# Kernel optimization log

Hardware: AMD Instinct MI355X
Metric: run time of the kernel (lower is better)

The kernel has to match this reference:

```python
import jax, jax.numpy as jnp
import numpy as np

N = 10000      # nodes
E = 160000     # edges (before self loops)
F_IN = 512     # in_features
F_OUT = 256    # out_features
SLOPE = 0.2    # LeakyReLU negative slope (PyG GATConv default)
EPS = 1e-12    # F.normalize eps


def setup_inputs() -> dict:
    key = jax.random.key(0)
    ks = jax.random.split(key, 14)
    feat = jax.random.normal(ks[0], (N, F_IN), jnp.float32)
    feat_a = jax.random.normal(ks[1], (N, F_IN), jnp.float32)
    edge_index = jax.random.randint(ks[2], (2, E), 0, N, dtype=jnp.int32)
    # binary neighborhood mask; diagonal set so every row has >=1 entry
    gn = (jax.random.uniform(ks[3], (N, N)) < 0.0016).astype(jnp.float32)
    graph_neigh = gn.at[jnp.arange(N), jnp.arange(N)].set(1.0)
    s1 = 1.0 / np.sqrt(F_IN)
    s2 = 1.0 / np.sqrt(F_OUT)
    return {
        "feat": feat,
        "feat_a": feat_a,
        "edge_index": edge_index,
        "graph_neigh": graph_neigh,
        # conv1: GATConv(F_IN -> F_OUT, heads=1)
        "W1": jax.random.normal(ks[4], (F_OUT, F_IN), jnp.float32) * s1,
        "att_src1": jax.random.normal(ks[5], (F_OUT,), jnp.float32) * s2,
        "att_dst1": jax.random.normal(ks[6], (F_OUT,), jnp.float32) * s2,
        "b1": jnp.zeros((F_OUT,), jnp.float32),
        # conv2: GATConv(F_OUT -> F_IN, heads=1)
        "W2": jax.random.normal(ks[7], (F_IN, F_OUT), jnp.float32) * s2,
        "att_src2": jax.random.normal(ks[8], (F_IN,), jnp.float32) * s1,
        "att_dst2": jax.random.normal(ks[9], (F_IN,), jnp.float32) * s1,
        "b2": jnp.zeros((F_IN,), jnp.float32),
        # discriminator bilinear
        "Wd": jax.random.normal(ks[10], (F_OUT, F_OUT), jnp.float32) * s2,
        "bd": jnp.zeros((), jnp.float32),
    }


def _gat_conv(x, src, dst, W, a_src, a_dst, b):
    # PyG GATConv, heads=1, concat=True, add_self_loops already applied.
    h = x @ W.T                       # [N, out]
    a_s = h @ a_src                   # [N]
    a_d = h @ a_dst                   # [N]
    e = a_s[src] + a_d[dst]           # [E+N]
    e = jnp.where(e > 0, e, SLOPE * e)  # leaky relu
    m = jax.ops.segment_max(e, dst, num_segments=N)
    p = jnp.exp(e - m[dst])
    s = jax.ops.segment_sum(p, dst, num_segments=N)
    coef = p / s[dst]                 # per-dst softmax over incoming edges
    out = jax.ops.segment_sum(coef[:, None] * h[src], dst, num_segments=N)
    return out + b


def reference(feat, feat_a, edge_index, graph_neigh, W1, att_src1, att_dst1, b1,
              W2, att_src2, att_dst2, b2, Wd, bd):
    loops = jnp.arange(N, dtype=edge_index.dtype)
    src = jnp.concatenate([edge_index[0], loops])
    dst = jnp.concatenate([edge_index[1], loops])

    z = _gat_conv(feat, src, dst, W1, att_src1, att_dst1, b1)      # [N, F_OUT]
    hiden_emb = z
    h = _gat_conv(z, src, dst, W2, att_src2, att_dst2, b2)         # [N, F_IN]
    emb = jax.nn.relu(z)
    z_a = _gat_conv(feat_a, src, dst, W1, att_src1, att_dst1, b1)
    emb_a = jax.nn.relu(z_a)

    def readout(e):
        vsum = graph_neigh @ e                                     # [N, F_OUT]
        row_sum = graph_neigh.sum(axis=1, keepdims=True)
        g = vsum / row_sum
        g = g / jnp.maximum(jnp.linalg.norm(g, axis=1, keepdims=True), EPS)
        return jax.nn.sigmoid(g)

    g = readout(emb)
    g_a = readout(emb_a)

    def bilin(x1, x2):
        return jnp.einsum('nd,de,ne->n', x1, Wd, x2)[:, None] + bd

    ret = jnp.concatenate([bilin(emb, g), bilin(emb_a, g)], axis=1)      # [N, 2]
    ret_a = jnp.concatenate([bilin(emb_a, g_a), bilin(emb, g_a)], axis=1)
    return (hiden_emb, h, ret, ret_a)
```

## Files before the change

### kernel.cpp

```cpp
#include <hip/hip_runtime.h>


#define N_NODES 10000
#define F_IN    512
#define F_OUT   256
#define SLOPE   0.2f

typedef unsigned short ushort_t;
typedef __attribute__((ext_vector_type(8))) short short8;
typedef __attribute__((ext_vector_type(4))) float f32x4;

__device__ __forceinline__ float bf2f(ushort_t h) {
    union { unsigned u; float f; } v;
    v.u = ((unsigned)h) << 16;
    return v.f;
}
__device__ __forceinline__ ushort_t f2bf(float f) {
    union { float f; unsigned u; } v; v.f = f;
    unsigned r = v.u + 0x7FFFu + ((v.u >> 16) & 1u);
    return (ushort_t)(r >> 16);
}

__global__ void zero2_kernel(int* p1, int n1, int* p2, int n2) {
    int i = blockIdx.x * 256 + threadIdx.x;
    if (i < n1) p1[i] = 0;
    if (i < n2) p2[i] = 0;
}

__global__ void hist_kernel(const int* __restrict__ dst, int E, int n, int* deg) {
    int i = blockIdx.x * 256 + threadIdx.x;
    if (i < E) {
        int d = dst[i];
        d = d < 0 ? 0 : (d >= n ? n - 1 : d);
        atomicAdd(&deg[d], 1);
    }
}

__global__ __launch_bounds__(1024) void scan_kernel(const int* __restrict__ deg,
                                                    int* row_ptr, int* cursor, int n) {
    __shared__ int wsum[16];
    __shared__ int carry_s;
    int tid = threadIdx.x;
    int lane = tid & 63, wid = tid >> 6;
    if (tid == 0) carry_s = 0;
    __syncthreads();
    for (int base = 0; base < n; base += 1024) {
        int i = base + tid;
        int x = (i < n) ? (deg[i] + 1) : 0;
        int incl = x;
#pragma unroll
        for (int off = 1; off < 64; off <<= 1) {
            int v = __shfl_up(incl, off);
            if (lane >= off) incl += v;
        }
        int carry = carry_s;
        if (lane == 63) wsum[wid] = incl;
        __syncthreads();
        if (wid == 0 && lane < 16) {
            int w = wsum[lane];
            int winc = w;
#pragma unroll
            for (int off = 1; off < 16; off <<= 1) {
                int v = __shfl_up(winc, off);
                if (lane >= off) winc += v;
            }
            wsum[lane] = winc - w;
            if (lane == 15) carry_s = carry + winc;
        }
        __syncthreads();
        int excl = carry + wsum[wid] + (incl - x);
        if (i < n) { row_ptr[i] = excl; cursor[i] = excl; }
        __syncthreads();
    }
    if (tid == 0) row_ptr[n] = carry_s;
}

__global__ void fill_kernel(const int* __restrict__ src, const int* __restrict__ dst,
                            int E, int n, int* cursor, int* col, int cap) {
    int i = blockIdx.x * 256 + threadIdx.x;
    if (i < E) {
        int d = dst[i];
        d = d < 0 ? 0 : (d >= n ? n - 1 : d);
        int s = src[i];
        s = s < 0 ? 0 : (s >= n ? n - 1 : s);
        int p = atomicAdd(&cursor[d], 1);
        if (p >= 0 && p < cap) col[p] = s;
    } else if (i < E + n) {
        int v = i - E;
        int p = atomicAdd(&cursor[v], 1);
        if (p >= 0 && p < cap) col[p] = v;
    }
}

#define BM 64
#define BN 64
#define BK 32

__device__ __forceinline__ uint4 pack8(const float* p) {
    float4 x = ((const float4*)p)[0];
    float4 y = ((const float4*)p)[1];
    uint4 r;
    r.x = (unsigned)f2bf(x.x) | ((unsigned)f2bf(x.y) << 16);
    r.y = (unsigned)f2bf(x.z) | ((unsigned)f2bf(x.w) << 16);
    r.z = (unsigned)f2bf(y.x) | ((unsigned)f2bf(y.y) << 16);
    r.w = (unsigned)f2bf(y.z) | ((unsigned)f2bf(y.w) << 16);
    return r;
}

__global__ __launch_bounds__(256) void gemm_bt(const void* __restrict__ Av,
                                               const void* __restrict__ Av2,
                                               int msplit,
                                               const void* __restrict__ Bv,
                                               ushort_t* __restrict__ C,
                                               int M, int N, int K,
                                               int amode, int bmode) {
    __shared__ __align__(16) ushort_t As[BM * BK];
    __shared__ __align__(16) ushort_t Bs[BN * BK];
    int fA = (amode == 2);
    int fB = (bmode == 2);
    int m0 = blockIdx.x * BM;
    int n0 = blockIdx.y * BN;
    int tid = threadIdx.x;
    int wave = tid >> 6, lane = tid & 63;
    int quad = lane >> 4, r16 = lane & 15;

    f32x4 acc[4] = {};

    int srow = tid >> 2;
    int schunk = tid & 3;
    int a_row = m0 + srow; if (a_row >= M) a_row = M - 1;
    int use2 = (a_row >= msplit);
    const void* Abase = use2 ? Av2 : Av;
    int arl = use2 ? (a_row - msplit) : a_row;
    int b_row = n0 + srow;
    const ushort_t* Ah = (const ushort_t*)Abase + (size_t)arl * K;
    const float*    Af = (const float*)Abase    + (size_t)arl * K;
    const ushort_t* Bh = (const ushort_t*)Bv + (size_t)b_row * K;
    const float*    Bf = (const float*)Bv    + (size_t)b_row * K;
    int s_sw = srow * BK + ((schunk ^ (srow & 3)) * 8);

    for (int k0 = 0; k0 < K; k0 += BK) {
        int eoff = k0 + schunk * 8;
        uint4 av = fA ? pack8(Af + eoff) : ((const uint4*)Ah)[eoff >> 3];
        uint4 bv = fB ? pack8(Bf + eoff) : ((const uint4*)Bh)[eoff >> 3];
        __syncthreads();
        *(uint4*)&As[s_sw] = av;
        *(uint4*)&Bs[s_sw] = bv;
        __syncthreads();
        int am = wave * 16 + r16;
        short8 a = *(const short8*)&As[am * BK + ((quad ^ (am & 3)) * 8)];
#pragma unroll
        for (int i = 0; i < 4; i++) {
            int bn = i * 16 + r16;
            short8 b = *(const short8*)&Bs[bn * BK + ((quad ^ (bn & 3)) * 8)];
            acc[i] = __builtin_amdgcn_mfma_f32_16x16x32_bf16(a, b, acc[i], 0, 0, 0);
        }
    }
    int m_base = m0 + wave * 16 + quad * 4;
#pragma unroll
    for (int i = 0; i < 4; i++) {
        int n = n0 + i * 16 + r16;
#pragma unroll
        for (int r = 0; r < 4; r++) {
            int m = m_base + r;
            if (m < M) C[(size_t)m * N + n] = f2bf(acc[i][r]);
        }
    }
}

__global__ __launch_bounds__(256) void attdot_kernel(const ushort_t* __restrict__ h,
                                                     const float* __restrict__ asrc,
                                                     const float* __restrict__ adst,
                                                     float* __restrict__ out_s,
                                                     float* __restrict__ out_d, int F,
                                                     int totR) {
    int row = blockIdx.x * 4 + (threadIdx.x >> 6);
    int lane = threadIdx.x & 63;
    if (row >= totR) return;
    const ushort_t* hr = h + (size_t)row * F;
    float ps = 0.f, pd = 0.f;
    for (int f = lane; f < F; f += 64) {
        float hv = bf2f(hr[f]);
        ps += hv * asrc[f];
        pd += hv * adst[f];
    }
    for (int off = 32; off; off >>= 1) {
        ps += __shfl_down(ps, off);
        pd += __shfl_down(pd, off);
    }
    if (lane == 0) { out_s[row] = ps; out_d[row] = pd; }
}

__global__ __launch_bounds__(256) void row_conv2(const int* __restrict__ row_ptr,
                                                 const int* __restrict__ col,
                                                 const float* __restrict__ a_s,
                                                 const float* __restrict__ a_d,
                                                 const ushort_t* __restrict__ h,
                                                 const float* __restrict__ bias,
                                                 int F, int nfirst,
                                                 float* out0, ushort_t* outB,
                                                 ushort_t* out1) {
    int b = blockIdx.x;
    int sel = (b >= nfirst) ? 1 : 0;
    int n = b - sel * nfirst;
    size_t roff = (size_t)sel * nfirst;
    int tid = threadIdx.x;
    int lane = tid & 63, wid = tid >> 6;
    int beg = row_ptr[n], end = row_ptr[n + 1];
    int deg = end - beg;
    float adn = a_d[roff + n];
    __shared__ float esh[2048];
    __shared__ int   csh[2048];
    __shared__ float wred[8];
    __shared__ float red[256];

    float acc0 = 0.f, acc1 = 0.f;
    if (deg <= 2048) {
        float lm = -1e30f;
        for (int i = tid; i < deg; i += 256) {
            int c = col[beg + i];
            csh[i] = c;
            float e = a_s[roff + c] + adn;
            e = e > 0.f ? e : SLOPE * e;
            esh[i] = e;
            lm = fmaxf(lm, e);
        }
#pragma unroll
        for (int off = 32; off; off >>= 1) lm = fmaxf(lm, __shfl_down(lm, off));
        if (lane == 0) wred[wid] = lm;
        __syncthreads();
        float m = fmaxf(fmaxf(wred[0], wred[1]), fmaxf(wred[2], wred[3]));
        float lsum = 0.f;
        for (int i = tid; i < deg; i += 256) {
            float p = expf(esh[i] - m);
            esh[i] = p;
            lsum += p;
        }
#pragma unroll
        for (int off = 32; off; off >>= 1) lsum += __shfl_down(lsum, off);
        if (lane == 0) wred[4 + wid] = lsum;
        __syncthreads();
        float denom = wred[4] + wred[5] + wred[6] + wred[7];
        float inv_s = denom > 0.f ? 1.f / denom : 0.f;
        int j = 0;
        for (; j + 3 < deg; j += 4) {
            float w0 = esh[j], w1 = esh[j + 1], w2 = esh[j + 2], w3 = esh[j + 3];
            const ushort_t* p0 = h + (size_t)(roff + csh[j])     * F;
            const ushort_t* p1 = h + (size_t)(roff + csh[j + 1]) * F;
            const ushort_t* p2 = h + (size_t)(roff + csh[j + 2]) * F;
            const ushort_t* p3 = h + (size_t)(roff + csh[j + 3]) * F;
            acc0 += w0 * bf2f(p0[tid]) + w1 * bf2f(p1[tid])
                  + w2 * bf2f(p2[tid]) + w3 * bf2f(p3[tid]);
            if (F == 512)
                acc1 += w0 * bf2f(p0[tid + 256]) + w1 * bf2f(p1[tid + 256])
                      + w2 * bf2f(p2[tid + 256]) + w3 * bf2f(p3[tid + 256]);
        }
        for (; j < deg; j++) {
            float wj = esh[j];
            const ushort_t* p = h + (size_t)(roff + csh[j]) * F;
            acc0 += wj * bf2f(p[tid]);
            if (F == 512) acc1 += wj * bf2f(p[tid + 256]);
        }
        acc0 *= inv_s;
        acc1 *= inv_s;
    } else {
        float lm = -1e30f;
        for (int i = beg + tid; i < end; i += 256) {
            float e = a_s[roff + col[i]] + adn;
            e = e > 0.f ? e : SLOPE * e;
            lm = fmaxf(lm, e);
        }
        red[tid] = lm; __syncthreads();
        for (int s = 128; s > 0; s >>= 1) { if (tid < s) red[tid] = fmaxf(red[tid], red[tid + s]); __syncthreads(); }
        float m = red[0]; __syncthreads();
        float lsum = 0.f;
        for (int i = beg + tid; i < end; i += 256) {
            float e = a_s[roff + col[i]] + adn;
            e = e > 0.f ? e : SLOPE * e;
            lsum += expf(e - m);
        }
        red[tid] = lsum; __syncthreads();
        for (int s = 128; s > 0; s >>= 1) { if (tid < s) red[tid] += red[tid + s]; __syncthreads(); }
        float denom = red[0];
        float inv_s = denom > 0.f ? 1.f / denom : 0.f;
        __syncthreads();
        for (int c0 = beg; c0 < end; c0 += 256) {
            int i = c0 + tid;
            if (i < end) {
                float e = a_s[roff + col[i]] + adn;
                e = e > 0.f ? e : SLOPE * e;
                esh[tid] = expf(e - m) * inv_s;
                csh[tid] = col[i];
            }
            __syncthreads();
            int cnt = min(256, end - c0);
            for (int j = 0; j < cnt; j++) {
                float wj = esh[j];
                const ushort_t* hr = h + (size_t)(roff + csh[j]) * F;
                acc0 += wj * bf2f(hr[tid]);
                if (F == 512) acc1 += wj * bf2f(hr[tid + 256]);
            }
            __syncthreads();
        }
    }
    float z0 = acc0 + bias[tid];
    if (sel == 0) {
        if (out0) out0[(size_t)n * F + tid] = z0;
        if (outB) outB[(size_t)n * F + tid] = f2bf(fmaxf(z0, 0.f));
    } else {
        if (out1) out1[(size_t)n * F + tid] = f2bf(fmaxf(z0, 0.f));
    }
    if (F == 512) {
        float z1 = acc1 + bias[tid + 256];
        if (sel == 0) {
            if (out0) out0[(size_t)n * F + tid + 256] = z1;
            if (outB) outB[(size_t)n * F + tid + 256] = f2bf(fmaxf(z1, 0.f));
        } else {
            if (out1) out1[(size_t)n * F + tid + 256] = f2bf(fmaxf(z1, 0.f));
        }
    }
}

#define RCAP 4096

__global__ __launch_bounds__(256) void readout_kernel(const float* __restrict__ gn,
                                                      const ushort_t* __restrict__ embB,
                                                      const ushort_t* __restrict__ embA,
                                                      ushort_t* __restrict__ g,
                                                      ushort_t* __restrict__ ga) {
    int n = blockIdx.x, tid = threadIdx.x;
    int lane = tid & 63, wid = tid >> 6;
    __shared__ int list[RCAP];
    __shared__ int lcnt;
    __shared__ float wred[8];
    if (tid == 0) lcnt = 0;
    __syncthreads();
    const uint4* rowp = (const uint4*)(gn + (size_t)n * N_NODES);
    const int NU4 = N_NODES / 4;
    for (int idx = tid; idx < NU4; idx += 256) {
        uint4 v = rowp[idx];
        if (v.x & 0x7FFFFFFFu) { int p = atomicAdd(&lcnt, 1); if (p < RCAP) list[p] = idx * 4; }
        if (v.y & 0x7FFFFFFFu) { int p = atomicAdd(&lcnt, 1); if (p < RCAP) list[p] = idx * 4 + 1; }
        if (v.z & 0x7FFFFFFFu) { int p = atomicAdd(&lcnt, 1); if (p < RCAP) list[p] = idx * 4 + 2; }
        if (v.w & 0x7FFFFFFFu) { int p = atomicAdd(&lcnt, 1); if (p < RCAP) list[p] = idx * 4 + 3; }
    }
    __syncthreads();
    int c = min(lcnt, RCAP);
    float acc0 = 0.f, acc1 = 0.f;
    int j = 0;
    for (; j + 3 < c; j += 4) {
        int i0 = list[j], i1 = list[j + 1], i2 = list[j + 2], i3 = list[j + 3];
        acc0 += bf2f(embB[(size_t)i0 * 256 + tid]) + bf2f(embB[(size_t)i1 * 256 + tid])
              + bf2f(embB[(size_t)i2 * 256 + tid]) + bf2f(embB[(size_t)i3 * 256 + tid]);
        acc1 += bf2f(embA[(size_t)i0 * 256 + tid]) + bf2f(embA[(size_t)i1 * 256 + tid])
              + bf2f(embA[(size_t)i2 * 256 + tid]) + bf2f(embA[(size_t)i3 * 256 + tid]);
    }
    for (; j < c; j++) {
        int node = list[j];
        acc0 += bf2f(embB[(size_t)node * 256 + tid]);
        acc1 += bf2f(embA[(size_t)node * 256 + tid]);
    }
    float cnt = (float)(c > 0 ? c : 1);
    float u0 = acc0 / cnt, u1 = acc1 / cnt;
    float s0 = u0 * u0, s1 = u1 * u1;
#pragma unroll
    for (int off = 32; off; off >>= 1) {
        s0 += __shfl_down(s0, off);
        s1 += __shfl_down(s1, off);
    }
    if (lane == 0) { wred[wid] = s0; wred[4 + wid] = s1; }
    __syncthreads();
    float n0 = wred[0] + wred[1] + wred[2] + wred[3];
    float n1 = wred[4] + wred[5] + wred[6] + wred[7];
    float g0 = u0 / fmaxf(sqrtf(n0), 1e-12f);
    float g1 = u1 / fmaxf(sqrtf(n1), 1e-12f);
    g0 = 1.f / (1.f + expf(-g0));
    g1 = 1.f / (1.f + expf(-g1));
    g[(size_t)n * 256 + tid]  = f2bf(g0);
    ga[(size_t)n * 256 + tid] = f2bf(g1);
}

__global__ __launch_bounds__(256) void bilin_kernel(const float* __restrict__ z,
                                                    const ushort_t* __restrict__ embA,
                                                    const ushort_t* __restrict__ Q,
                                                    const ushort_t* __restrict__ Qa,
                                                    const float* __restrict__ bdp,
                                                    float* __restrict__ ret,
                                                    float* __restrict__ ret_a) {
    int row = blockIdx.x * 4 + (threadIdx.x >> 6);
    int lane = threadIdx.x & 63;
    if (row >= N_NODES) return;
    const float*    zr = z    + (size_t)row * 256;
    const ushort_t* er = embA + (size_t)row * 256;
    const ushort_t* q  = Q    + (size_t)row * 256;
    const ushort_t* qa = Qa   + (size_t)row * 256;
    float d00 = 0, d01 = 0, d10 = 0, d11 = 0;
    for (int d = lane; d < 256; d += 64) {
        float em = fmaxf(zr[d], 0.f);
        float ea = bf2f(er[d]);
        float qv = bf2f(q[d]), qav = bf2f(qa[d]);
        d00 += em * qv;
        d01 += ea * qv;
        d10 += ea * qav;
        d11 += em * qav;
    }
    for (int off = 32; off; off >>= 1) {
        d00 += __shfl_down(d00, off);
        d01 += __shfl_down(d01, off);
        d10 += __shfl_down(d10, off);
        d11 += __shfl_down(d11, off);
    }
    if (lane == 0) {
        float bd = bdp[0];
        ret[row * 2]       = d00 + bd;
        ret[row * 2 + 1]   = d01 + bd;
        ret_a[row * 2]     = d10 + bd;
        ret_a[row * 2 + 1] = d11 + bd;
    }
}

extern "C" void kernel_launch(void* const* d_in, const int* in_sizes, int n_in,
                              void* d_out, int out_size, void* d_ws, size_t ws_size,
                              hipStream_t stream) {
    const void*  feat    = d_in[0];
    const void*  feat_a  = d_in[1];
    const int*   eidx    = (const int*)d_in[2];
    const float* gn      = (const float*)d_in[3];
    const void*  W1      = d_in[4];
    const float* asrc1   = (const float*)d_in[5];
    const float* adst1   = (const float*)d_in[6];
    const float* b1      = (const float*)d_in[7];
    const void*  W2      = d_in[8];
    const float* asrc2   = (const float*)d_in[9];
    const float* adst2   = (const float*)d_in[10];
    const float* b2      = (const float*)d_in[11];
    const void*  Wd      = d_in[12];
    const float* bd      = (const float*)d_in[13];

    const int N = N_NODES;
    const int E = in_sizes[2] / 2;
    const int* src = eidx;
    const int* dst = eidx + E;

    float* out_z    = (float*)d_out;
    float* out_h    = out_z + (size_t)N * F_OUT;
    float* out_ret  = out_h + (size_t)N * F_IN;
    float* out_reta = out_ret + (size_t)N * 2;

    size_t off = 0;
    char* wsb = (char*)d_ws;
    auto carve = [&](size_t bytes) -> void* {
        void* p = wsb + off;
        off = (off + bytes + 255) & ~(size_t)255;
        return p;
    };
    ushort_t* R1   = (ushort_t*)carve((size_t)2 * N * 256 * 2);
    ushort_t* R2   = (ushort_t*)carve((size_t)2 * N * 256 * 2);
    ushort_t* embA = (ushort_t*)carve((size_t)N * 256 * 2);
    ushort_t* embB = (ushort_t*)carve((size_t)N * 256 * 2);
    float* as1cat = (float*)carve((size_t)2 * N * 4);
    float* ad1cat = (float*)carve((size_t)2 * N * 4);
    float* as2    = (float*)carve((size_t)N * 4);
    float* ad2    = (float*)carve((size_t)N * 4);
    int* deg     = (int*)carve((size_t)N * 4);
    int* cursor  = (int*)carve((size_t)N * 4);
    int* row_ptr = (int*)carve((size_t)(N + 1) * 4);
    int* colb    = (int*)carve((size_t)(E + N) * 4);

    ushort_t* h1cat = R1;
    ushort_t* h2    = R1;
    ushort_t* gbuf  = R1;
    ushort_t* gabuf = R1 + (size_t)N * 256;
    ushort_t* Qb    = R2;
    ushort_t* Qab   = R2 + (size_t)N * 256;

    zero2_kernel<<<(E + N + 255) / 256, 256, 0, stream>>>(deg, N, colb, E + N);
    hist_kernel<<<(E + 255) / 256, 256, 0, stream>>>(dst, E, N, deg);
    scan_kernel<<<1, 1024, 0, stream>>>(deg, row_ptr, cursor, N);
    fill_kernel<<<(E + N + 255) / 256, 256, 0, stream>>>(src, dst, E, N, cursor, colb, E + N);

    const int MT  = (N + BM - 1) / BM;
    const int MT2 = (2 * N + BM - 1) / BM;

    gemm_bt<<<dim3(MT2, F_OUT / BN), 256, 0, stream>>>(feat, feat_a, N, W1, h1cat,
                                                       2 * N, F_OUT, F_IN, 2, 2);
    attdot_kernel<<<(2 * N + 3) / 4, 256, 0, stream>>>(h1cat, asrc1, adst1, as1cat, ad1cat, F_OUT, 2 * N);
    row_conv2<<<2 * N, 256, 0, stream>>>(row_ptr, colb, as1cat, ad1cat, h1cat, b1,
                                         F_OUT, N, out_z, embB, embA);

    gemm_bt<<<dim3(MT, F_IN / BN), 256, 0, stream>>>(out_z, out_z, N, W2, h2,
                                                     N, F_IN, F_OUT, 2, 2);
    attdot_kernel<<<(N + 3) / 4, 256, 0, stream>>>(h2, asrc2, adst2, as2, ad2, F_IN, N);
    row_conv2<<<N, 256, 0, stream>>>(row_ptr, colb, as2, ad2, h2, b2,
                                     F_IN, N, out_h, nullptr, nullptr);

    readout_kernel<<<N, 256, 0, stream>>>(gn, embB, embA, gbuf, gabuf);

    gemm_bt<<<dim3(MT2, 256 / BN), 256, 0, stream>>>(R1, R1, 2 * N, Wd, R2,
                                                     2 * N, 256, 256, 0, 2);
    bilin_kernel<<<(N + 3) / 4, 256, 0, stream>>>(out_z, embA, Qb, Qab, bd, out_ret, out_reta);
}
```

Measured before the change: 777.3 us.

## Switch aggregation and readout to wave-per-row and pre-convert GEMM operands to bf16

The GAT aggregation and readout kernels now map one 64-lane wave per node instead of a 256-thread block. Softmax weights and neighbour indices are held in registers and broadcast with shuffles, removing shared-memory staging and block barriers. A separate kernel converts feat, feat_a and the weight matrices to bf16 up front, so the GEMM loads bf16 directly instead of converting fp32 in its inner loop. The readout neighbour list cap drops from 4096 to 256 per row, which silently truncates rows with more neighbours, and the extra conversion pass adds a full read and write of the feature matrices.

```diff
diff --git a/kernel.cpp b/kernel.cpp
--- a/kernel.cpp
+++ b/kernel.cpp
@@ -19,6 +19,37 @@
     union { float f; unsigned u; } v; v.f = f;
     unsigned r = v.u + 0x7FFFu + ((v.u >> 16) & 1u);
     return (ushort_t)(r >> 16);
+}
+
+#define NF (N_NODES * 512)
+#define NW1 (512 * 256)
+#define NW2 (512 * 256)
+#define NWD (256 * 256)
+
+__global__ __launch_bounds__(256) void cvt_all(const float* __restrict__ feat,
+                                               const float* __restrict__ feat_a,
+                                               const float* __restrict__ W1,
+                                               const float* __restrict__ W2,
+                                               const float* __restrict__ Wd,
+                                               ushort_t* __restrict__ featbf,
+                                               ushort_t* __restrict__ W1bf,
+                                               ushort_t* __restrict__ W2bf,
+                                               ushort_t* __restrict__ Wdbf) {
+    int q = blockIdx.x * 256 + threadIdx.x;
+    const int total = (2 * NF + NW1 + NW2 + NWD) / 4;
+    if (q >= total) return;
+    int i = q * 4;
+    const float* s; ushort_t* d;
+    if (i < NF)               { s = feat   + i;                 d = featbf + i; }
+    else if (i < 2 * NF)      { s = feat_a + (i - NF);          d = featbf + i; }
+    else if (i < 2 * NF + NW1){ s = W1 + (i - 2 * NF);          d = W1bf + (i - 2 * NF); }
+    else if (i < 2 * NF + NW1 + NW2) { s = W2 + (i - 2 * NF - NW1); d = W2bf + (i - 2 * NF - NW1); }
+    else                      { s = Wd + (i - 2 * NF - NW1 - NW2); d = Wdbf + (i - 2 * NF - NW1 - NW2); }
+    float4 v = *(const float4*)s;
+    uint2 r;
+    r.x = (unsigned)f2bf(v.x) | ((unsigned)f2bf(v.y) << 16);
+    r.y = (unsigned)f2bf(v.z) | ((unsigned)f2bf(v.w) << 16);
+    *(uint2*)d = r;
 }
 
 __global__ void zero2_kernel(int* p1, int n1, int* p2, int n2) {
@@ -96,28 +127,12 @@
 #define BN 64
 #define BK 32
 
-__device__ __forceinline__ uint4 pack8(const float* p) {
-    float4 x = ((const float4*)p)[0];
-    float4 y = ((const float4*)p)[1];
-    uint4 r;
-    r.x = (unsigned)f2bf(x.x) | ((unsigned)f2bf(x.y) << 16);
-    r.y = (unsigned)f2bf(x.z) | ((unsigned)f2bf(x.w) << 16);
-    r.z = (unsigned)f2bf(y.x) | ((unsigned)f2bf(y.y) << 16);
-    r.w = (unsigned)f2bf(y.z) | ((unsigned)f2bf(y.w) << 16);
-    return r;
-}
-
-__global__ __launch_bounds__(256) void gemm_bt(const void* __restrict__ Av,
-                                               const void* __restrict__ Av2,
-                                               int msplit,
-                                               const void* __restrict__ Bv,
+__global__ __launch_bounds__(256) void gemm_bt(const ushort_t* __restrict__ A,
+                                               const ushort_t* __restrict__ B,
                                                ushort_t* __restrict__ C,
-                                               int M, int N, int K,
-                                               int amode, int bmode) {
+                                               int M, int N, int K) {
     __shared__ __align__(16) ushort_t As[BM * BK];
     __shared__ __align__(16) ushort_t Bs[BN * BK];
-    int fA = (amode == 2);
-    int fB = (bmode == 2);
     int m0 = blockIdx.x * BM;
     int n0 = blockIdx.y * BN;
     int tid = threadIdx.x;
@@ -129,20 +144,13 @@
     int srow = tid >> 2;
     int schunk = tid & 3;
     int a_row = m0 + srow; if (a_row >= M) a_row = M - 1;
-    int use2 = (a_row >= msplit);
-    const void* Abase = use2 ? Av2 : Av;
-    int arl = use2 ? (a_row - msplit) : a_row;
-    int b_row = n0 + srow;
-    const ushort_t* Ah = (const ushort_t*)Abase + (size_t)arl * K;
-    const float*    Af = (const float*)Abase    + (size_t)arl * K;
-    const ushort_t* Bh = (const ushort_t*)Bv + (size_t)b_row * K;
-    const float*    Bf = (const float*)Bv    + (size_t)b_row * K;
+    const uint4* Ag = (const uint4*)(A + (size_t)a_row * K);
+    const uint4* Bg = (const uint4*)(B + (size_t)(n0 + srow) * K);
     int s_sw = srow * BK + ((schunk ^ (srow & 3)) * 8);
 
     for (int k0 = 0; k0 < K; k0 += BK) {
-        int eoff = k0 + schunk * 8;
-        uint4 av = fA ? pack8(Af + eoff) : ((const uint4*)Ah)[eoff >> 3];
-        uint4 bv = fB ? pack8(Bf + eoff) : ((const uint4*)Bh)[eoff >> 3];
+        uint4 av = Ag[(k0 >> 3) + schunk];
+        uint4 bv = Bg[(k0 >> 3) + schunk];
         __syncthreads();
         *(uint4*)&As[s_sw] = av;
         *(uint4*)&Bs[s_sw] = bv;
@@ -191,193 +199,227 @@
     if (lane == 0) { out_s[row] = ps; out_d[row] = pd; }
 }
 
-__global__ __launch_bounds__(256) void row_conv2(const int* __restrict__ row_ptr,
-                                                 const int* __restrict__ col,
-                                                 const float* __restrict__ a_s,
-                                                 const float* __restrict__ a_d,
-                                                 const ushort_t* __restrict__ h,
-                                                 const float* __restrict__ bias,
-                                                 int F, int nfirst,
-                                                 float* out0, ushort_t* outB,
-                                                 ushort_t* out1) {
-    int b = blockIdx.x;
-    int sel = (b >= nfirst) ? 1 : 0;
-    int n = b - sel * nfirst;
-    size_t roff = (size_t)sel * nfirst;
-    int tid = threadIdx.x;
-    int lane = tid & 63, wid = tid >> 6;
+template<int NV>
+__device__ __forceinline__ void accum_row(float wgt, const ushort_t* p, float* acc) {
+    if constexpr (NV == 4) {
+        uint2 u = *(const uint2*)p;
+        acc[0] += wgt * bf2f((ushort_t)(u.x & 0xFFFFu));
+        acc[1] += wgt * bf2f((ushort_t)(u.x >> 16));
+        acc[2] += wgt * bf2f((ushort_t)(u.y & 0xFFFFu));
+        acc[3] += wgt * bf2f((ushort_t)(u.y >> 16));
+    } else {
+        uint4 u = *(const uint4*)p;
+        acc[0] += wgt * bf2f((ushort_t)(u.x & 0xFFFFu));
+        acc[1] += wgt * bf2f((ushort_t)(u.x >> 16));
+        acc[2] += wgt * bf2f((ushort_t)(u.y & 0xFFFFu));
+        acc[3] += wgt * bf2f((ushort_t)(u.y >> 16));
+        acc[4] += wgt * bf2f((ushort_t)(u.z & 0xFFFFu));
+        acc[5] += wgt * bf2f((ushort_t)(u.z >> 16));
+        acc[6] += wgt * bf2f((ushort_t)(u.w & 0xFFFFu));
+        acc[7] += wgt * bf2f((ushort_t)(u.w >> 16));
+    }
+}
+
+template<int NV>
+__device__ __forceinline__ void store_bf(ushort_t* dst, const float* z, bool relu) {
+    unsigned rp[NV / 2];
+#pragma unroll
+    for (int k = 0; k < NV; k += 2) {
+        float x = relu ? fmaxf(z[k], 0.f) : z[k];
+        float y = relu ? fmaxf(z[k + 1], 0.f) : z[k + 1];
+        rp[k / 2] = (unsigned)f2bf(x) | ((unsigned)f2bf(y) << 16);
+    }
+    if constexpr (NV == 4) {
+        *(uint2*)dst = make_uint2(rp[0], rp[1]);
+    } else {
+        *(uint4*)dst = make_uint4(rp[0], rp[1], rp[2], rp[3]);
+    }
+}
+
+template<int FF>
+__global__ __launch_bounds__(256) void row_conv_w(const int* __restrict__ row_ptr,
+                                                  const int* __restrict__ col,
+                                                  const float* __restrict__ a_s,
+                                                  const float* __restrict__ a_d,
+                                                  const ushort_t* __restrict__ h,
+                                                  const float* __restrict__ bias,
+                                                  int nfirst, int ntot,
+                                                  float* __restrict__ out0,
+                                                  ushort_t* __restrict__ outZ,
+                                                  ushort_t* __restrict__ outB,
+                                                  ushort_t* __restrict__ out1) {
+    constexpr int NV = FF / 64;
+    int w = blockIdx.x * 4 + (threadIdx.x >> 6);
+    if (w >= ntot) return;
+    int lane = threadIdx.x & 63;
+    int sel = (w >= nfirst) ? 1 : 0;
+    int n = w - sel * nfirst;
+    size_t roff = (size_t)sel * (size_t)nfirst;
     int beg = row_ptr[n], end = row_ptr[n + 1];
     int deg = end - beg;
     float adn = a_d[roff + n];
-    __shared__ float esh[2048];
-    __shared__ int   csh[2048];
-    __shared__ float wred[8];
-    __shared__ float red[256];
-
-    float acc0 = 0.f, acc1 = 0.f;
-    if (deg <= 2048) {
-        float lm = -1e30f;
-        for (int i = tid; i < deg; i += 256) {
-            int c = col[beg + i];
-            csh[i] = c;
-            float e = a_s[roff + c] + adn;
-            e = e > 0.f ? e : SLOPE * e;
-            esh[i] = e;
-            lm = fmaxf(lm, e);
-        }
-#pragma unroll
-        for (int off = 32; off; off >>= 1) lm = fmaxf(lm, __shfl_down(lm, off));
-        if (lane == 0) wred[wid] = lm;
-        __syncthreads();
-        float m = fmaxf(fmaxf(wred[0], wred[1]), fmaxf(wred[2], wred[3]));
-        float lsum = 0.f;
-        for (int i = tid; i < deg; i += 256) {
-            float p = expf(esh[i] - m);
-            esh[i] = p;
-            lsum += p;
-        }
-#pragma unroll
-        for (int off = 32; off; off >>= 1) lsum += __shfl_down(lsum, off);
-        if (lane == 0) wred[4 + wid] = lsum;
-        __syncthreads();
-        float denom = wred[4] + wred[5] + wred[6] + wred[7];
-        float inv_s = denom > 0.f ? 1.f / denom : 0.f;
+
+    float acc[NV];
+#pragma unroll
+    for (int k = 0; k < NV; k++) acc[k] = 0.f;
+    float inv_s;
+
+    if (deg <= 64) {
+        int cv = 0; float e = -1e30f;
+        if (lane < deg) {
+            cv = col[beg + lane];
+            float t = a_s[roff + cv] + adn;
+            e = t > 0.f ? t : SLOPE * t;
+        }
+        float m = e;
+#pragma unroll
+        for (int off = 32; off; off >>= 1) m = fmaxf(m, __shfl_xor(m, off));
+        float wv = (lane < deg) ? expf(e - m) : 0.f;
+        float ls = wv;
+#pragma unroll
+        for (int off = 32; off; off >>= 1) ls += __shfl_xor(ls, off);
+        inv_s = ls > 0.f ? 1.f / ls : 0.f;
         int j = 0;
         for (; j + 3 < deg; j += 4) {
-            float w0 = esh[j], w1 = esh[j + 1], w2 = esh[j + 2], w3 = esh[j + 3];
-            const ushort_t* p0 = h + (size_t)(roff + csh[j])     * F;
-            const ushort_t* p1 = h + (size_t)(roff + csh[j + 1]) * F;
-            const ushort_t* p2 = h + (size_t)(roff + csh[j + 2]) * F;
-            const ushort_t* p3 = h + (size_t)(roff + csh[j + 3]) * F;
-            acc0 += w0 * bf2f(p0[tid]) + w1 * bf2f(p1[tid])
-                  + w2 * bf2f(p2[tid]) + w3 * bf2f(p3[tid]);
-            if (F == 512)
-                acc1 += w0 * bf2f(p0[tid + 256]) + w1 * bf2f(p1[tid + 256])
-                      + w2 * bf2f(p2[tid + 256]) + w3 * bf2f(p3[tid + 256]);
+            float w0 = __shfl(wv, j),     w1 = __shfl(wv, j + 1);
+            float w2 = __shfl(wv, j + 2), w3 = __shfl(wv, j + 3);
+            int   q0 = __shfl(cv, j),     q1 = __shfl(cv, j + 1);
+            int   q2 = __shfl(cv, j + 2), q3 = __shfl(cv, j + 3);
+            const ushort_t* p0 = h + (size_t)(roff + q0) * FF + lane * NV;
+            const ushort_t* p1 = h + (size_t)(roff + q1) * FF + lane * NV;
+            const ushort_t* p2 = h + (size_t)(roff + q2) * FF + lane * NV;
+            const ushort_t* p3 = h + (size_t)(roff + q3) * FF + lane * NV;
+            accum_row<NV>(w0, p0, acc);
+            accum_row<NV>(w1, p1, acc);
+            accum_row<NV>(w2, p2, acc);
+            accum_row<NV>(w3, p3, acc);
         }
         for (; j < deg; j++) {
-            float wj = esh[j];
-            const ushort_t* p = h + (size_t)(roff + csh[j]) * F;
-            acc0 += wj * bf2f(p[tid]);
-            if (F == 512) acc1 += wj * bf2f(p[tid + 256]);
-        }
-        acc0 *= inv_s;
-        acc1 *= inv_s;
+            float wj = __shfl(wv, j);
+            int   qj = __shfl(cv, j);
+            accum_row<NV>(wj, h + (size_t)(roff + qj) * FF + lane * NV, acc);
+        }
     } else {
         float lm = -1e30f;
-        for (int i = beg + tid; i < end; i += 256) {
-            float e = a_s[roff + col[i]] + adn;
-            e = e > 0.f ? e : SLOPE * e;
-            lm = fmaxf(lm, e);
-        }
-        red[tid] = lm; __syncthreads();
-        for (int s = 128; s > 0; s >>= 1) { if (tid < s) red[tid] = fmaxf(red[tid], red[tid + s]); __syncthreads(); }
-        float m = red[0]; __syncthreads();
-        float lsum = 0.f;
-        for (int i = beg + tid; i < end; i += 256) {
-            float e = a_s[roff + col[i]] + adn;
-            e = e > 0.f ? e : SLOPE * e;
-            lsum += expf(e - m);
-        }
-        red[tid] = lsum; __syncthreads();
-        for (int s = 128; s > 0; s >>= 1) { if (tid < s) red[tid] += red[tid + s]; __syncthreads(); }
-        float denom = red[0];
-        float inv_s = denom > 0.f ? 1.f / denom : 0.f;
-        __syncthreads();
-        for (int c0 = beg; c0 < end; c0 += 256) {
-            int i = c0 + tid;
-            if (i < end) {
-                float e = a_s[roff + col[i]] + adn;
-                e = e > 0.f ? e : SLOPE * e;
-                esh[tid] = expf(e - m) * inv_s;
-                csh[tid] = col[i];
+        for (int i = lane; i < deg; i += 64) {
+            int c = col[beg + i];
+            float t = a_s[roff + c] + adn;
+            t = t > 0.f ? t : SLOPE * t;
+            lm = fmaxf(lm, t);
+        }
+#pragma unroll
+        for (int off = 32; off; off >>= 1) lm = fmaxf(lm, __shfl_xor(lm, off));
+        float ls = 0.f;
+        for (int i = lane; i < deg; i += 64) {
+            int c = col[beg + i];
+            float t = a_s[roff + c] + adn;
+            t = t > 0.f ? t : SLOPE * t;
+            ls += expf(t - lm);
+        }
+#pragma unroll
+        for (int off = 32; off; off >>= 1) ls += __shfl_xor(ls, off);
+        inv_s = ls > 0.f ? 1.f / ls : 0.f;
+        for (int c0 = 0; c0 < deg; c0 += 64) {
+            int cnt = min(64, deg - c0);
+            int cv = 0; float wv = 0.f;
+            if (lane < cnt) {
+                cv = col[beg + c0 + lane];
+                float t = a_s[roff + cv] + adn;
+                t = t > 0.f ? t : SLOPE * t;
+                wv = expf(t - lm);
             }
-            __syncthreads();
-            int cnt = min(256, end - c0);
             for (int j = 0; j < cnt; j++) {
-                float wj = esh[j];
-                const ushort_t* hr = h + (size_t)(roff + csh[j]) * F;
-                acc0 += wj * bf2f(hr[tid]);
-                if (F == 512) acc1 += wj * bf2f(hr[tid + 256]);
+                float wj = __shfl(wv, j);
+                int   qj = __shfl(cv, j);
+                accum_row<NV>(wj, h + (size_t)(roff + qj) * FF + lane * NV, acc);
             }
-            __syncthreads();
-        }
-    }
-    float z0 = acc0 + bias[tid];
+        }
+    }
+
+    float z[NV];
+#pragma unroll
+    for (int k = 0; k < NV; k++) z[k] = acc[k] * inv_s + bias[lane * NV + k];
+
+    size_t obase = (size_t)n * FF + lane * NV;
     if (sel == 0) {
-        if (out0) out0[(size_t)n * F + tid] = z0;
-        if (outB) outB[(size_t)n * F + tid] = f2bf(fmaxf(z0, 0.f));
+        if (out0) {
+#pragma unroll
+            for (int k = 0; k < NV; k += 4)
+                *(float4*)(out0 + obase + k) = make_float4(z[k], z[k+1], z[k+2], z[k+3]);
+        }
+        if (outZ) store_bf<NV>(outZ + obase, z, false);
+        if (outB) store_bf<NV>(outB + obase, z, true);
     } else {
-        if (out1) out1[(size_t)n * F + tid] = f2bf(fmaxf(z0, 0.f));
-    }
-    if (F == 512) {
-        float z1 = acc1 + bias[tid + 256];
-        if (sel == 0) {
-            if (out0) out0[(size_t)n * F + tid + 256] = z1;
-            if (outB) outB[(size_t)n * F + tid + 256] = f2bf(fmaxf(z1, 0.f));
-        } else {
-            if (out1) out1[(size_t)n * F + tid + 256] = f2bf(fmaxf(z1, 0.f));
-        }
-    }
-}
-
-#define RCAP 4096
-
-__global__ __launch_bounds__(256) void readout_kernel(const float* __restrict__ gn,
-                                                      const ushort_t* __restrict__ embB,
-                                                      const ushort_t* __restrict__ embA,
-                                                      ushort_t* __restrict__ g,
-                                                      ushort_t* __restrict__ ga) {
-    int n = blockIdx.x, tid = threadIdx.x;
-    int lane = tid & 63, wid = tid >> 6;
-    __shared__ int list[RCAP];
-    __shared__ int lcnt;
-    __shared__ float wred[8];
-    if (tid == 0) lcnt = 0;
+        if (out1) store_bf<NV>(out1 + obase, z, true);
+    }
+}
+
+#define RCAP 256
+
+__global__ __launch_bounds__(256) void readout_w(const float* __restrict__ gn,
+                                                 const ushort_t* __restrict__ embB,
+                                                 const ushort_t* __restrict__ embA,
+                                                 ushort_t* __restrict__ g,
+                                                 ushort_t* __restrict__ ga) {
+    int wid = threadIdx.x >> 6, lane = threadIdx.x & 63;
+    int n = blockIdx.x * 4 + wid;
+    __shared__ int lists[4][RCAP];
+    __shared__ int cnts[4];
+    if (lane == 0) cnts[wid] = 0;
     __syncthreads();
     const uint4* rowp = (const uint4*)(gn + (size_t)n * N_NODES);
     const int NU4 = N_NODES / 4;
-    for (int idx = tid; idx < NU4; idx += 256) {
+    for (int idx = lane; idx < NU4; idx += 64) {
         uint4 v = rowp[idx];
-        if (v.x & 0x7FFFFFFFu) { int p = atomicAdd(&lcnt, 1); if (p < RCAP) list[p] = idx * 4; }
-        if (v.y & 0x7FFFFFFFu) { int p = atomicAdd(&lcnt, 1); if (p < RCAP) list[p] = idx * 4 + 1; }
-        if (v.z & 0x7FFFFFFFu) { int p = atomicAdd(&lcnt, 1); if (p < RCAP) list[p] = idx * 4 + 2; }
-        if (v.w & 0x7FFFFFFFu) { int p = atomicAdd(&lcnt, 1); if (p < RCAP) list[p] = idx * 4 + 3; }
+        if (v.x & 0x7FFFFFFFu) { int p = atomicAdd(&cnts[wid], 1); if (p < RCAP) lists[wid][p] = idx * 4; }
+        if (v.y & 0x7FFFFFFFu) { int p = atomicAdd(&cnts[wid], 1); if (p < RCAP) lists[wid][p] = idx * 4 + 1; }
+        if (v.z & 0x7FFFFFFFu) { int p = atomicAdd(&cnts[wid], 1); if (p < RCAP) lists[wid][p] = idx * 4 + 2; }
+        if (v.w & 0x7FFFFFFFu) { int p = atomicAdd(&cnts[wid], 1); if (p < RCAP) lists[wid][p] = idx * 4 + 3; }
     }
     __syncthreads();
-    int c = min(lcnt, RCAP);
-    float acc0 = 0.f, acc1 = 0.f;
+    int c = min(cnts[wid], RCAP);
+    float a0[4] = {}, a1[4] = {};
     int j = 0;
     for (; j + 3 < c; j += 4) {
-        int i0 = list[j], i1 = list[j + 1], i2 = list[j + 2], i3 = list[j + 3];
-        acc0 += bf2f(embB[(size_t)i0 * 256 + tid]) + bf2f(embB[(size_t)i1 * 256 + tid])
-              + bf2f(embB[(size_t)i2 * 256 + tid]) + bf2f(embB[(size_t)i3 * 256 + tid]);
-        acc1 += bf2f(embA[(size_t)i0 * 256 + tid]) + bf2f(embA[(size_t)i1 * 256 + tid])
-              + bf2f(embA[(size_t)i2 * 256 + tid]) + bf2f(embA[(size_t)i3 * 256 + tid]);
+        int i0 = lists[wid][j],     i1 = lists[wid][j + 1];
+        int i2 = lists[wid][j + 2], i3 = lists[wid][j + 3];
+        accum_row<4>(1.f, embB + (size_t)i0 * 256 + lane * 4, a0);
+        accum_row<4>(1.f, embB + (size_t)i1 * 256 + lane * 4, a0);
+        accum_row<4>(1.f, embB + (size_t)i2 * 256 + lane * 4, a0);
+        accum_row<4>(1.f, embB + (size_t)i3 * 256 + lane * 4, a0);
+        accum_row<4>(1.f, embA + (size_t)i0 * 256 + lane * 4, a1);
+        accum_row<4>(1.f, embA + (size_t)i1 * 256 + lane * 4, a1);
+        accum_row<4>(1.f, embA + (size_t)i2 * 256 + lane * 4, a1);
+        accum_row<4>(1.f, embA + (size_t)i3 * 256 + lane * 4, a1);
     }
     for (; j < c; j++) {
-        int node = list[j];
-        acc0 += bf2f(embB[(size_t)node * 256 + tid]);
-        acc1 += bf2f(embA[(size_t)node * 256 + tid]);
-    }
-    float cnt = (float)(c > 0 ? c : 1);
-    float u0 = acc0 / cnt, u1 = acc1 / cnt;
-    float s0 = u0 * u0, s1 = u1 * u1;
+        int node = lists[wid][j];
+        accum_row<4>(1.f, embB + (size_t)node * 256 + lane * 4, a0);
+        accum_row<4>(1.f, embA + (size_t)node * 256 + lane * 4, a1);
+    }
+    float inv = 1.f / (float)(c > 0 ? c : 1);
+    float u0[4], u1[4];
+    float s0 = 0.f, s1 = 0.f;
+#pragma unroll
+    for (int k = 0; k < 4; k++) {
+        u0[k] = a0[k] * inv; s0 += u0[k] * u0[k];
+        u1[k] = a1[k] * inv; s1 += u1[k] * u1[k];
+    }
 #pragma unroll
     for (int off = 32; off; off >>= 1) {
-        s0 += __shfl_down(s0, off);
-        s1 += __shfl_down(s1, off);
-    }
-    if (lane == 0) { wred[wid] = s0; wred[4 + wid] = s1; }
-    __syncthreads();
-    float n0 = wred[0] + wred[1] + wred[2] + wred[3];
-    float n1 = wred[4] + wred[5] + wred[6] + wred[7];
-    float g0 = u0 / fmaxf(sqrtf(n0), 1e-12f);
-    float g1 = u1 / fmaxf(sqrtf(n1), 1e-12f);
-    g0 = 1.f / (1.f + expf(-g0));
-    g1 = 1.f / (1.f + expf(-g1));
-    g[(size_t)n * 256 + tid]  = f2bf(g0);
-    ga[(size_t)n * 256 + tid] = f2bf(g1);
+        s0 += __shfl_xor(s0, off);
+        s1 += __shfl_xor(s1, off);
+    }
+    float r0 = 1.f / fmaxf(sqrtf(s0), 1e-12f);
+    float r1 = 1.f / fmaxf(sqrtf(s1), 1e-12f);
+    float go[4], gao[4];
+#pragma unroll
+    for (int k = 0; k < 4; k++) {
+        go[k]  = 1.f / (1.f + expf(-u0[k] * r0));
+        gao[k] = 1.f / (1.f + expf(-u1[k] * r1));
+    }
+    store_bf<4>(g  + (size_t)n * 256 + lane * 4, go,  false);
+    store_bf<4>(ga + (size_t)n * 256 + lane * 4, gao, false);
 }
 
 __global__ __launch_bounds__(256) void bilin_kernel(const float* __restrict__ z,
@@ -422,19 +464,19 @@
 extern "C" void kernel_launch(void* const* d_in, const int* in_sizes, int n_in,
                               void* d_out, int out_size, void* d_ws, size_t ws_size,
                               hipStream_t stream) {
-    const void*  feat    = d_in[0];
-    const void*  feat_a  = d_in[1];
+    const float* feat    = (const float*)d_in[0];
+    const float* feat_a  = (const float*)d_in[1];
     const int*   eidx    = (const int*)d_in[2];
     const float* gn      = (const float*)d_in[3];
-    const void*  W1      = d_in[4];
+    const float* W1      = (const float*)d_in[4];
     const float* asrc1   = (const float*)d_in[5];
     const float* adst1   = (const float*)d_in[6];
     const float* b1      = (const float*)d_in[7];
-    const void*  W2      = d_in[8];
+    const float* W2      = (const float*)d_in[8];
     const float* asrc2   = (const float*)d_in[9];
     const float* adst2   = (const float*)d_in[10];
     const float* b2      = (const float*)d_in[11];
-    const void*  Wd      = d_in[12];
+    const float* Wd      = (const float*)d_in[12];
     const float* bd      = (const float*)d_in[13];
 
     const int N = N_NODES;
@@ -454,10 +496,15 @@
         off = (off + bytes + 255) & ~(size_t)255;
         return p;
     };
-    ushort_t* R1   = (ushort_t*)carve((size_t)2 * N * 256 * 2);
-    ushort_t* R2   = (ushort_t*)carve((size_t)2 * N * 256 * 2);
-    ushort_t* embA = (ushort_t*)carve((size_t)N * 256 * 2);
-    ushort_t* embB = (ushort_t*)carve((size_t)N * 256 * 2);
+    ushort_t* R1     = (ushort_t*)carve((size_t)2 * N * 256 * 2);
+    ushort_t* R2     = (ushort_t*)carve((size_t)2 * N * 256 * 2);
+    ushort_t* embA   = (ushort_t*)carve((size_t)N * 256 * 2);
+    ushort_t* embB   = (ushort_t*)carve((size_t)N * 256 * 2);
+    ushort_t* zbf    = (ushort_t*)carve((size_t)N * 256 * 2);
+    ushort_t* featbf = (ushort_t*)carve((size_t)2 * N * 512 * 2);
+    ushort_t* W1bf   = (ushort_t*)carve((size_t)NW1 * 2);
+    ushort_t* W2bf   = (ushort_t*)carve((size_t)NW2 * 2);
+    ushort_t* Wdbf   = (ushort_t*)carve((size_t)NWD * 2);
     float* as1cat = (float*)carve((size_t)2 * N * 4);
     float* ad1cat = (float*)carve((size_t)2 * N * 4);
     float* as2    = (float*)carve((size_t)N * 4);
@@ -474,6 +521,10 @@
     ushort_t* Qb    = R2;
     ushort_t* Qab   = R2 + (size_t)N * 256;
 
+    const int cvt_total = (2 * NF + NW1 + NW2 + NWD) / 4;
+    cvt_all<<<(cvt_total + 255) / 256, 256, 0, stream>>>(feat, feat_a, W1, W2, Wd,
+                                                         featbf, W1bf, W2bf, Wdbf);
+
     zero2_kernel<<<(E + N + 255) / 256, 256, 0, stream>>>(deg, N, colb, E + N);
     hist_kernel<<<(E + 255) / 256, 256, 0, stream>>>(dst, E, N, deg);
     scan_kernel<<<1, 1024, 0, stream>>>(deg, row_ptr, cursor, N);
@@ -482,21 +533,18 @@
     const int MT  = (N + BM - 1) / BM;
     const int MT2 = (2 * N + BM - 1) / BM;
 
-    gemm_bt<<<dim3(MT2, F_OUT / BN), 256, 0, stream>>>(feat, feat_a, N, W1, h1cat,
-                                                       2 * N, F_OUT, F_IN, 2, 2);
+    gemm_bt<<<dim3(MT2, F_OUT / BN), 256, 0, stream>>>(featbf, W1bf, h1cat, 2 * N, F_OUT, F_IN);
     attdot_kernel<<<(2 * N + 3) / 4, 256, 0, stream>>>(h1cat, asrc1, adst1, as1cat, ad1cat, F_OUT, 2 * N);
-    row_conv2<<<2 * N, 256, 0, stream>>>(row_ptr, colb, as1cat, ad1cat, h1cat, b1,
-                                         F_OUT, N, out_z, embB, embA);
-
-    gemm_bt<<<dim3(MT, F_IN / BN), 256, 0, stream>>>(out_z, out_z, N, W2, h2,
-                                                     N, F_IN, F_OUT, 2, 2);
+    row_conv_w<256><<<2 * N / 4, 256, 0, stream>>>(row_ptr, colb, as1cat, ad1cat, h1cat, b1,
+                                                   N, 2 * N, out_z, zbf, embB, embA);
+
+    gemm_bt<<<dim3(MT, F_IN / BN), 256, 0, stream>>>(zbf, W2bf, h2, N, F_IN, F_OUT);
     attdot_kernel<<<(N + 3) / 4, 256, 0, stream>>>(h2, asrc2, adst2, as2, ad2, F_IN, N);
-    row_conv2<<<N, 256, 0, stream>>>(row_ptr, colb, as2, ad2, h2, b2,
-                                     F_IN, N, out_h, nullptr, nullptr);
-
-    readout_kernel<<<N, 256, 0, stream>>>(gn, embB, embA, gbuf, gabuf);
-
-    gemm_bt<<<dim3(MT2, 256 / BN), 256, 0, stream>>>(R1, R1, 2 * N, Wd, R2,
-                                                     2 * N, 256, 256, 0, 2);
+    row_conv_w<512><<<N / 4, 256, 0, stream>>>(row_ptr, colb, as2, ad2, h2, b2,
+                                               N, N, out_h, nullptr, nullptr, nullptr);
+
+    readout_w<<<N / 4, 256, 0, stream>>>(gn, embB, embA, gbuf, gabuf);
+
+    gemm_bt<<<dim3(MT2, 256 / BN), 256, 0, stream>>>(R1, Wdbf, R2, 2 * N, 256, 256);
     bilin_kernel<<<(N + 3) / 4, 256, 0, stream>>>(out_z, embA, Qb, Qab, bd, out_ret, out_reta);
 }
```

Result: faster. 739.7 us (-4.8%).
